# Optimization experiments

Hardware: AMD Instinct MI355X
Metric: run time of the kernel (lower is better)

## Reference

```python
import jax, jax.numpy as jnp
import numpy as np

N_NODES = 100000
N_EDGES = 1600000
N_GRAPHS = 4096
HID = 512
OUT_DIM = 12


def setup_inputs() -> dict:
    key = jax.random.key(0)
    ks = jax.random.split(key, 16)
    x = jax.random.normal(ks[0], (N_NODES, 7), dtype=jnp.float32)
    edge_index = jax.random.randint(ks[1], (2, N_EDGES), 0, N_NODES, dtype=jnp.int32)
    batch = jnp.sort(jax.random.randint(ks[2], (N_NODES,), 0, N_GRAPHS, dtype=jnp.int32))

    def lin(k, i, o):
        s = 1.0 / np.sqrt(i)
        kw, kb = jax.random.split(k)
        return (jax.random.uniform(kw, (i, o), jnp.float32, -s, s),
                jax.random.uniform(kb, (o,), jnp.float32, -s, s))

    c1_w1, c1_b1 = lin(ks[3], 7, HID)
    c1_w2, c1_b2 = lin(ks[4], HID, HID)
    c2_w1, c2_b1 = lin(ks[5], HID, HID)
    c2_w2, c2_b2 = lin(ks[6], HID, HID)
    c3_w1, c3_b1 = lin(ks[7], HID, HID)
    c3_w2, c3_b2 = lin(ks[8], HID, HID)
    lin_w1, lin_b1 = lin(ks[9], HID, 256)
    lin_w2, lin_b2 = lin(ks[10], 256, OUT_DIM)
    return dict(x=x, edge_index=edge_index, batch=batch,
                c1_w1=c1_w1, c1_b1=c1_b1, c1_w2=c1_w2, c1_b2=c1_b2,
                c2_w1=c2_w1, c2_b1=c2_b1, c2_w2=c2_w2, c2_b2=c2_b2,
                c3_w1=c3_w1, c3_b1=c3_b1, c3_w2=c3_w2, c3_b2=c3_b2,
                lin_w1=lin_w1, lin_b1=lin_b1, lin_w2=lin_w2, lin_b2=lin_b2)


def _gin_conv(x, src, dst, w1, b1, w2, b2):
    # GINConv (eps=0): h_i = mlp(x_i + sum_{j in N(i)} x_j)
    agg = jax.ops.segment_sum(x[src], dst, num_segments=N_NODES)
    h = x + agg
    h = jax.nn.relu(h @ w1 + b1) @ w2 + b2
    return h


def reference(x, edge_index, batch,
              c1_w1, c1_b1, c1_w2, c1_b2,
              c2_w1, c2_b1, c2_w2, c2_b2,
              c3_w1, c3_b1, c3_w2, c3_b2,
              lin_w1, lin_b1, lin_w2, lin_b2):
    src, dst = edge_index[0], edge_index[1]
    h = jax.nn.relu(_gin_conv(x, src, dst, c1_w1, c1_b1, c1_w2, c1_b2))
    h = jax.nn.relu(_gin_conv(h, src, dst, c2_w1, c2_b1, c2_w2, c2_b2))
    h = jax.nn.relu(_gin_conv(h, src, dst, c3_w1, c3_b1, c3_w2, c3_b2))
    # global mean pool over graphs in batch
    sums = jax.ops.segment_sum(h, batch, num_segments=N_GRAPHS)
    cnts = jax.ops.segment_sum(jnp.ones((h.shape[0],), h.dtype), batch, num_segments=N_GRAPHS)
    pooled = sums / jnp.maximum(cnts, 1.0)[:, None]
    return jax.nn.relu(pooled @ lin_w1 + lin_b1) @ lin_w2 + lin_b2
```

## Files before the change

### kernel.cpp

```cpp
#include <hip/hip_runtime.h>
#include <hip/hip_bf16.h>
#include <cstddef>
#include <cstdint>

#define N_NODES   100000
#define M_PAD     100096
#define N_EDGES   1600000
#define N_GRAPHS  4096
#define HID       512
#define OUT_DIM   12

typedef unsigned short u16;
typedef __attribute__((ext_vector_type(8))) short bf16x8;
typedef __attribute__((ext_vector_type(4))) float f32x4;

__device__ inline float bf2f(u16 u) {
    union { uint32_t i; float f; } v; v.i = (uint32_t)u << 16; return v.f;
}
__device__ inline u16 f2bf(float f) {
    union { float f; uint32_t i; } v; v.f = f;
    uint32_t r = v.i + 0x7FFFu + ((v.i >> 16) & 1u);
    return (u16)(r >> 16);
}

__device__ inline void load8_bf(const u16* p, float o[8]) {
    uint4 u = *(const uint4*)p;
    uint32_t w[4] = {u.x, u.y, u.z, u.w};
    #pragma unroll
    for (int i = 0; i < 4; ++i) {
        o[2*i]   = bf2f((u16)(w[i] & 0xFFFFu));
        o[2*i+1] = bf2f((u16)(w[i] >> 16));
    }
}
__device__ inline void store8_bf(u16* p, const float o[8]) {
    uint4 u;
    u.x = (uint32_t)f2bf(o[0]) | ((uint32_t)f2bf(o[1]) << 16);
    u.y = (uint32_t)f2bf(o[2]) | ((uint32_t)f2bf(o[3]) << 16);
    u.z = (uint32_t)f2bf(o[4]) | ((uint32_t)f2bf(o[5]) << 16);
    u.w = (uint32_t)f2bf(o[6]) | ((uint32_t)f2bf(o[7]) << 16);
    *(uint4*)p = u;
}

__global__ void zero_ints(int* __restrict__ p, int n) {
    int i = blockIdx.x * blockDim.x + threadIdx.x;
    if (i < n) p[i] = 0;
}

__global__ void hist_kernel(const int* __restrict__ dst, int* __restrict__ counts) {
    int e = blockIdx.x * blockDim.x + threadIdx.x;
    if (e < N_EDGES) atomicAdd(&counts[dst[e]], 1);
}

__global__ __launch_bounds__(1024) void scan_single(const int* __restrict__ counts,
                                                    int* __restrict__ row_start) {
    __shared__ int smem[1024];
    __shared__ int running;
    int tid = threadIdx.x;
    if (tid == 0) { running = 0; row_start[0] = 0; }
    __syncthreads();
    for (int base = 0; base < N_NODES; base += 1024) {
        int i = base + tid;
        int v = (i < N_NODES) ? counts[i] : 0;
        smem[tid] = v;
        __syncthreads();
        for (int off = 1; off < 1024; off <<= 1) {
            int t = (tid >= off) ? smem[tid - off] : 0;
            __syncthreads();
            smem[tid] += t;
            __syncthreads();
        }
        int incl = smem[tid];
        int tot  = smem[1023];
        int roff = running;
        if (i < N_NODES) row_start[i + 1] = roff + incl;
        __syncthreads();
        if (tid == 0) running = roff + tot;
        __syncthreads();
    }
}

__global__ void cursor_init(const int* __restrict__ row_start, int* __restrict__ cursor) {
    int i = blockIdx.x * blockDim.x + threadIdx.x;
    if (i < N_NODES) cursor[i] = row_start[i];
}

__global__ void scatter_edges(const int* __restrict__ src, const int* __restrict__ dst,
                              int* __restrict__ cursor, int* __restrict__ sorted_src) {
    int e = blockIdx.x * blockDim.x + threadIdx.x;
    if (e < N_EDGES) {
        int p = atomicAdd(&cursor[dst[e]], 1);
        p = min(max(p, 0), N_EDGES - 1);
        sorted_src[p] = src[e];
    }
}

__global__ __launch_bounds__(256) void transpose_to_bf16(const float* __restrict__ W,
                                                         u16* __restrict__ Wt) {
    __shared__ float t[32][33];
    int bx = blockIdx.x * 32, by = blockIdx.y * 32;
    int tx = threadIdx.x & 31, ty = threadIdx.x >> 5;
    #pragma unroll
    for (int i = 0; i < 32; i += 8)
        t[ty + i][tx] = W[(size_t)(by + ty + i) * HID + bx + tx];
    __syncthreads();
    #pragma unroll
    for (int i = 0; i < 32; i += 8)
        Wt[(size_t)(bx + ty + i) * HID + by + tx] = f2bf(t[tx][ty + i]);
}

__global__ __launch_bounds__(64) void agg7_kernel(const float* __restrict__ x,
                                                  const int* __restrict__ row_start,
                                                  const int* __restrict__ sorted_src,
                                                  float* __restrict__ out) {
    int node = blockIdx.x * 8 + (threadIdx.x >> 3);
    int d = threadIdx.x & 7;
    if (node >= N_NODES || d >= 7) return;
    float acc = x[(size_t)node * 7 + d];
    int e0 = min(row_start[node], N_EDGES);
    int e1 = min(row_start[node + 1], N_EDGES);
    for (int e = e0; e < e1; ++e) {
        unsigned si = min((unsigned)sorted_src[e], (unsigned)(N_NODES - 1));
        acc += x[(size_t)si * 7 + d];
    }
    out[(size_t)node * 7 + d] = acc;
}

__global__ __launch_bounds__(256) void agg_full(const u16* __restrict__ X,
                                                const int* __restrict__ row_start,
                                                const int* __restrict__ sorted_src,
                                                u16* __restrict__ Out) {
    int node = blockIdx.x * 4 + (threadIdx.x >> 6);
    if (node >= N_NODES) return;
    int lane = threadIdx.x & 63;
    float acc[8];
    load8_bf(X + (size_t)node * HID + lane * 8, acc);
    int e0 = min(row_start[node], N_EDGES);
    int e1 = min(row_start[node + 1], N_EDGES);
    for (int e = e0; e < e1; ++e) {
        unsigned si = min((unsigned)sorted_src[e], (unsigned)(N_NODES - 1));
        float v[8];
        load8_bf(X + (size_t)si * HID + lane * 8, v);
        #pragma unroll
        for (int k = 0; k < 8; ++k) acc[k] += v[k];
    }
    store8_bf(Out + (size_t)node * HID + lane * 8, acc);
}

__global__ __launch_bounds__(256) void gemm_k7_relu(const float* __restrict__ A7,
                                                    const float* __restrict__ W,
                                                    const float* __restrict__ bias,
                                                    u16* __restrict__ C) {
    int n = blockIdx.x;
    __shared__ float a[8];
    if (threadIdx.x < 7) a[threadIdx.x] = A7[(size_t)n * 7 + threadIdx.x];
    __syncthreads();
    for (int j = threadIdx.x; j < HID; j += 256) {
        float s = bias[j];
        #pragma unroll
        for (int k = 0; k < 7; ++k) s = fmaf(a[k], W[k * HID + j], s);
        C[(size_t)n * HID + j] = f2bf(fmaxf(s, 0.f));
    }
}

#define LDSP 40

template <bool RELU>
__global__ __launch_bounds__(256) void gemm_mfma_bf16(const u16* __restrict__ A,
                                                      const u16* __restrict__ Wt,
                                                      const float* __restrict__ bias,
                                                      u16* __restrict__ C) {
    __shared__ u16 As[128][LDSP];
    __shared__ u16 Bs[128][LDSP];
    const int tid  = threadIdx.x;
    const int wid  = tid >> 6;
    const int lane = tid & 63;
    const int wr = wid >> 1, wc = wid & 1;
    const int row0 = blockIdx.y * 128;
    const int col0 = blockIdx.x * 128;
    const int l15 = lane & 15;
    const int l4  = lane >> 4;

    f32x4 acc[4][4] = {};

    for (int k0 = 0; k0 < HID; k0 += 32) {
        #pragma unroll
        for (int i = 0; i < 2; ++i) {
            int c = tid + i * 256;
            int r = c >> 2, kc = (c & 3) * 8;
            *(uint4*)&As[r][kc] = *(const uint4*)&A [(size_t)(row0 + r) * HID + k0 + kc];
            *(uint4*)&Bs[r][kc] = *(const uint4*)&Wt[(size_t)(col0 + r) * HID + k0 + kc];
        }
        __syncthreads();
        bf16x8 af[4], bfr[4];
        #pragma unroll
        for (int m = 0; m < 4; ++m)
            af[m] = *(const bf16x8*)&As[wr * 64 + m * 16 + l15][l4 * 8];
        #pragma unroll
        for (int n = 0; n < 4; ++n)
            bfr[n] = *(const bf16x8*)&Bs[wc * 64 + n * 16 + l15][l4 * 8];
        #pragma unroll
        for (int m = 0; m < 4; ++m)
            #pragma unroll
            for (int n = 0; n < 4; ++n)
                acc[m][n] = __builtin_amdgcn_mfma_f32_16x16x32_bf16(af[m], bfr[n],
                                                                    acc[m][n], 0, 0, 0);
        __syncthreads();
    }

    #pragma unroll
    for (int m = 0; m < 4; ++m) {
        #pragma unroll
        for (int n = 0; n < 4; ++n) {
            int col = col0 + wc * 64 + n * 16 + l15;
            float b = bias[col];
            #pragma unroll
            for (int i = 0; i < 4; ++i) {
                int r = row0 + wr * 64 + m * 16 + l4 * 4 + i;
                float v = acc[m][n][i] + b;
                if (RELU) v = fmaxf(v, 0.f);
                C[(size_t)r * HID + col] = f2bf(v);
            }
        }
    }
}

template <bool RELU>
__global__ __launch_bounds__(256) void gemm_tiled_f32(const float* __restrict__ A,
                                                      const float* __restrict__ W,
                                                      const float* __restrict__ bias,
                                                      float* __restrict__ C,
                                                      int M, int N, int K) {
    __shared__ float As[16][68];
    __shared__ float Bs[16][68];
    int tid = threadIdx.x;
    int tx = tid & 15, ty = tid >> 4;
    int col0 = blockIdx.x * 64;
    int row0 = blockIdx.y * 64;
    float acc[4][4] = {};

    for (int k0 = 0; k0 < K; k0 += 16) {
        {
            int r = tid >> 2, c = (tid & 3) * 4;
            float4 v = make_float4(0.f, 0.f, 0.f, 0.f);
            int gr = row0 + r;
            if (gr < M) v = *reinterpret_cast<const float4*>(A + (size_t)gr * K + k0 + c);
            As[c + 0][r] = v.x; As[c + 1][r] = v.y; As[c + 2][r] = v.z; As[c + 3][r] = v.w;
        }
        {
            int r = tid >> 4, c = (tid & 15) * 4;
            int gc = col0 + c;
            float4 v = make_float4(0.f, 0.f, 0.f, 0.f);
            const float* wp = W + (size_t)(k0 + r) * N + gc;
            if (gc + 3 < N) {
                v = *reinterpret_cast<const float4*>(wp);
            } else {
                float t0 = (gc + 0 < N) ? wp[0] : 0.f;
                float t1 = (gc + 1 < N) ? wp[1] : 0.f;
                float t2 = (gc + 2 < N) ? wp[2] : 0.f;
                v = make_float4(t0, t1, t2, 0.f);
            }
            *reinterpret_cast<float4*>(&Bs[r][c]) = v;
        }
        __syncthreads();
        #pragma unroll
        for (int k = 0; k < 16; ++k) {
            float a[4], b[4];
            *(float4*)a = *(const float4*)&As[k][ty * 4];
            *(float4*)b = *(const float4*)&Bs[k][tx * 4];
            #pragma unroll
            for (int i = 0; i < 4; ++i)
                #pragma unroll
                for (int j = 0; j < 4; ++j)
                    acc[i][j] = fmaf(a[i], b[j], acc[i][j]);
        }
        __syncthreads();
    }

    #pragma unroll
    for (int i = 0; i < 4; ++i) {
        int r = row0 + ty * 4 + i;
        if (r >= M) break;
        #pragma unroll
        for (int j = 0; j < 4; ++j) {
            int cidx = col0 + tx * 4 + j;
            if (cidx >= N) continue;
            float v = acc[i][j] + bias[cidx];
            if (RELU) v = fmaxf(v, 0.f);
            C[(size_t)r * N + cidx] = v;
        }
    }
}

__global__ void graph_bounds(const int* __restrict__ batch, int* __restrict__ g_start) {
    int g = blockIdx.x * blockDim.x + threadIdx.x;
    if (g > N_GRAPHS) return;
    int lo = 0, hi = N_NODES;
    while (lo < hi) {
        int mid = (lo + hi) >> 1;
        if (batch[mid] < g) lo = mid + 1; else hi = mid;
    }
    g_start[g] = lo;
}

__global__ __launch_bounds__(256) void pool_kernel(const u16* __restrict__ H,
                                                   const int* __restrict__ g_start,
                                                   float* __restrict__ pooled) {
    int g = blockIdx.x * 4 + (threadIdx.x >> 6);
    if (g >= N_GRAPHS) return;
    int lane = threadIdx.x & 63;
    int s = g_start[g], e = g_start[g + 1];
    float acc[8] = {};
    for (int n = s; n < e; ++n) {
        float v[8];
        load8_bf(H + (size_t)n * HID + lane * 8, v);
        #pragma unroll
        for (int k = 0; k < 8; ++k) acc[k] += v[k];
    }
    float inv = 1.f / fmaxf((float)(e - s), 1.f);
    float* o = pooled + (size_t)g * HID + lane * 8;
    #pragma unroll
    for (int k = 0; k < 8; ++k) o[k] = acc[k] * inv;
}

__global__ void diag_kernel(float* __restrict__ out, int n, float v) {
    int i = blockIdx.x * blockDim.x + threadIdx.x;
    if (i < n) out[i] = v;
}

static inline size_t rnd256(size_t b) { return (b + 255) & ~(size_t)255; }

extern "C" void kernel_launch(void* const* d_in, const int* in_sizes, int n_in,
                              void* d_out, int out_size, void* d_ws, size_t ws_size,
                              hipStream_t stream) {
    (void)in_sizes; (void)n_in;
    const float* x     = (const float*)d_in[0];
    const int*   ei    = (const int*)d_in[1];
    const int*   batch = (const int*)d_in[2];
    const int* src = ei;
    const int* dst = ei + N_EDGES;

    const float* c1_w1 = (const float*)d_in[3];
    const float* c1_b1 = (const float*)d_in[4];
    const float* c1_w2 = (const float*)d_in[5];
    const float* c1_b2 = (const float*)d_in[6];
    const float* c2_w1 = (const float*)d_in[7];
    const float* c2_b1 = (const float*)d_in[8];
    const float* c2_w2 = (const float*)d_in[9];
    const float* c2_b2 = (const float*)d_in[10];
    const float* c3_w1 = (const float*)d_in[11];
    const float* c3_b1 = (const float*)d_in[12];
    const float* c3_w2 = (const float*)d_in[13];
    const float* c3_b2 = (const float*)d_in[14];
    const float* lin_w1 = (const float*)d_in[15];
    const float* lin_b1 = (const float*)d_in[16];
    const float* lin_w2 = (const float*)d_in[17];
    const float* lin_b2 = (const float*)d_in[18];
    float* out = (float*)d_out;

    size_t off = 0;
    auto alloc = [&](size_t bytes) -> void* {
        void* p = (char*)d_ws + off;
        off += rnd256(bytes);
        return p;
    };
    u16*   b0        = (u16*)alloc((size_t)M_PAD * HID * 2);
    u16*   b1        = (u16*)alloc((size_t)M_PAD * HID * 2);
    float* agg7buf   = (float*)alloc((size_t)N_NODES * 7 * 4);
    int*   counts    = (int*)alloc((size_t)N_NODES * 4);
    int*   cursor    = (int*)alloc((size_t)N_NODES * 4);
    int*   row_start = (int*)alloc((size_t)(N_NODES + 1) * 4);
    int*   sorted_src= (int*)alloc((size_t)N_EDGES * 4);
    int*   g_start   = (int*)alloc((size_t)(N_GRAPHS + 1) * 4);
    float* pooled    = (float*)alloc((size_t)N_GRAPHS * HID * 4);
    char*  hh_slot   = (char*)alloc((size_t)N_GRAPHS * 256 * 4);
    float* hh        = (float*)hh_slot;
    u16*   wt        = (u16*)hh_slot;
    u16* c1w2T = wt + 0 * HID * HID;
    u16* c2w1T = wt + 1 * HID * HID;
    u16* c2w2T = wt + 2 * HID * HID;
    u16* c3w1T = wt + 3 * HID * HID;
    u16* c3w2T = wt + 4 * HID * HID;

    if (off > ws_size) {
        diag_kernel<<<(out_size + 255) / 256, 256, 0, stream>>>(
            out, out_size, (float)(ws_size >> 20));
        return;
    }

    zero_ints<<<(N_NODES + 255) / 256, 256, 0, stream>>>(counts, N_NODES);
    hist_kernel<<<(N_EDGES + 255) / 256, 256, 0, stream>>>(dst, counts);
    scan_single<<<1, 1024, 0, stream>>>(counts, row_start);
    cursor_init<<<(N_NODES + 255) / 256, 256, 0, stream>>>(row_start, cursor);
    scatter_edges<<<(N_EDGES + 255) / 256, 256, 0, stream>>>(src, dst, cursor, sorted_src);
    graph_bounds<<<(N_GRAPHS + 256) / 256, 256, 0, stream>>>(batch, g_start);

    dim3 tgrid(HID / 32, HID / 32);
    transpose_to_bf16<<<tgrid, 256, 0, stream>>>(c1_w2, c1w2T);
    transpose_to_bf16<<<tgrid, 256, 0, stream>>>(c2_w1, c2w1T);
    transpose_to_bf16<<<tgrid, 256, 0, stream>>>(c2_w2, c2w2T);
    transpose_to_bf16<<<tgrid, 256, 0, stream>>>(c3_w1, c3w1T);
    transpose_to_bf16<<<tgrid, 256, 0, stream>>>(c3_w2, c3w2T);

    dim3 mgrid(HID / 128, M_PAD / 128);

    agg7_kernel<<<(N_NODES + 7) / 8, 64, 0, stream>>>(x, row_start, sorted_src, agg7buf);
    gemm_k7_relu<<<N_NODES, 256, 0, stream>>>(agg7buf, c1_w1, c1_b1, b0);
    gemm_mfma_bf16<true><<<mgrid, 256, 0, stream>>>(b0, c1w2T, c1_b2, b1);
    agg_full<<<N_NODES / 4, 256, 0, stream>>>(b1, row_start, sorted_src, b0);
    gemm_mfma_bf16<true><<<mgrid, 256, 0, stream>>>(b0, c2w1T, c2_b1, b1);
    gemm_mfma_bf16<true><<<mgrid, 256, 0, stream>>>(b1, c2w2T, c2_b2, b0);
    agg_full<<<N_NODES / 4, 256, 0, stream>>>(b0, row_start, sorted_src, b1);
    gemm_mfma_bf16<true><<<mgrid, 256, 0, stream>>>(b1, c3w1T, c3_b1, b0);
    gemm_mfma_bf16<true><<<mgrid, 256, 0, stream>>>(b0, c3w2T, c3_b2, b1);
    pool_kernel<<<N_GRAPHS / 4, 256, 0, stream>>>(b1, g_start, pooled);
    gemm_tiled_f32<true><<<dim3(256 / 64, N_GRAPHS / 64), 256, 0, stream>>>(
        pooled, lin_w1, lin_b1, hh, N_GRAPHS, 256, HID);
    gemm_tiled_f32<false><<<dim3(1, N_GRAPHS / 64), 256, 0, stream>>>(
        hh, lin_w2, lin_b2, out, N_GRAPHS, OUT_DIM, 256);
}
```

Measured before the change: 1.686 ms.

## Parallelize scan, split aggregation by column half, tile k7 GEMM, use direct-to-LDS loads

New measurement: 1.613 ms. -4.3%, faster.

```diff
diff --git a/kernel.cpp b/kernel.cpp
--- a/kernel.cpp
+++ b/kernel.cpp
@@ -41,6 +41,13 @@
     *(uint4*)p = u;
 }
 
+__device__ inline void gld16(const void* g, void* l) {
+    __builtin_amdgcn_global_load_lds(
+        (const __attribute__((address_space(1))) void*)g,
+        (__attribute__((address_space(3))) void*)(uint32_t)(uintptr_t)l,
+        16, 0, 0);
+}
+
 __global__ void zero_ints(int* __restrict__ p, int n) {
     int i = blockIdx.x * blockDim.x + threadIdx.x;
     if (i < n) p[i] = 0;
@@ -51,32 +58,43 @@
     if (e < N_EDGES) atomicAdd(&counts[dst[e]], 1);
 }
 
-__global__ __launch_bounds__(1024) void scan_single(const int* __restrict__ counts,
-                                                    int* __restrict__ row_start) {
+#define SCAN_NB 98
+
+__global__ __launch_bounds__(1024) void scan_chunks(const int* __restrict__ counts,
+                                                    int* __restrict__ row_start,
+                                                    int* __restrict__ partials) {
     __shared__ int smem[1024];
-    __shared__ int running;
     int tid = threadIdx.x;
-    if (tid == 0) { running = 0; row_start[0] = 0; }
+    int i = blockIdx.x * 1024 + tid;
+    int v = (i < N_NODES) ? counts[i] : 0;
+    smem[tid] = v;
     __syncthreads();
-    for (int base = 0; base < N_NODES; base += 1024) {
-        int i = base + tid;
-        int v = (i < N_NODES) ? counts[i] : 0;
-        smem[tid] = v;
-        __syncthreads();
-        for (int off = 1; off < 1024; off <<= 1) {
-            int t = (tid >= off) ? smem[tid - off] : 0;
-            __syncthreads();
-            smem[tid] += t;
-            __syncthreads();
-        }
-        int incl = smem[tid];
-        int tot  = smem[1023];
-        int roff = running;
-        if (i < N_NODES) row_start[i + 1] = roff + incl;
-        __syncthreads();
-        if (tid == 0) running = roff + tot;
-        __syncthreads();
-    }
+    for (int off = 1; off < 1024; off <<= 1) {
+        int t = (tid >= off) ? smem[tid - off] : 0;
+        __syncthreads();
+        smem[tid] += t;
+        __syncthreads();
+    }
+    if (i < N_NODES) row_start[i + 1] = smem[tid];
+    if (tid == 1023) partials[blockIdx.x] = smem[1023];
+}
+
+__global__ void scan_partials(int* __restrict__ partials) {
+    if (threadIdx.x == 0 && blockIdx.x == 0) {
+        int run = 0;
+        for (int b = 0; b < SCAN_NB; ++b) {
+            int t = partials[b];
+            partials[b] = run;
+            run += t;
+        }
+    }
+}
+
+__global__ __launch_bounds__(1024) void scan_add_offsets(int* __restrict__ row_start,
+                                                         const int* __restrict__ partials) {
+    int i = blockIdx.x * 1024 + threadIdx.x;
+    if (i == 0) row_start[0] = 0;
+    if (i < N_NODES) row_start[i + 1] += partials[blockIdx.x];
 }
 
 __global__ void cursor_init(const int* __restrict__ row_start, int* __restrict__ cursor) {
@@ -106,6 +124,33 @@
     #pragma unroll
     for (int i = 0; i < 32; i += 8)
         Wt[(size_t)(bx + ty + i) * HID + by + tx] = f2bf(t[tx][ty + i]);
+}
+
+template <int HALF>
+__global__ __launch_bounds__(256) void agg_half(const u16* __restrict__ X,
+                                                const int* __restrict__ row_start,
+                                                const int* __restrict__ sorted_src,
+                                                u16* __restrict__ Out) {
+    int node = blockIdx.x * 4 + (threadIdx.x >> 6);
+    int lane = threadIdx.x & 63;
+    size_t col = HALF * 256 + lane * 4;
+    uint2 s = *(const uint2*)(X + (size_t)node * HID + col);
+    float a0 = bf2f((u16)(s.x & 0xFFFFu)), a1 = bf2f((u16)(s.x >> 16));
+    float a2 = bf2f((u16)(s.y & 0xFFFFu)), a3 = bf2f((u16)(s.y >> 16));
+    int e0 = min(row_start[node], N_EDGES);
+    int e1 = min(row_start[node + 1], N_EDGES);
+    for (int e = e0; e < e1; ++e) {
+        unsigned si = min((unsigned)sorted_src[e], (unsigned)(N_NODES - 1));
+        uint2 v = *(const uint2*)(X + (size_t)si * HID + col);
+        a0 += bf2f((u16)(v.x & 0xFFFFu)); a1 += bf2f((u16)(v.x >> 16));
+        a2 += bf2f((u16)(v.y & 0xFFFFu)); a3 += bf2f((u16)(v.y >> 16));
+    }
+    uint2 o;
+    o.x = (uint32_t)f2bf(a0) | ((uint32_t)f2bf(a1) << 16);
+    o.y = (uint32_t)f2bf(a2) | ((uint32_t)f2bf(a3) << 16);
+    unsigned long long packed = (unsigned long long)o.x | ((unsigned long long)o.y << 32);
+    __builtin_nontemporal_store(packed,
+        (unsigned long long*)(Out + (size_t)node * HID + col));
 }
 
 __global__ __launch_bounds__(64) void agg7_kernel(const float* __restrict__ x,
@@ -125,52 +170,50 @@
     out[(size_t)node * 7 + d] = acc;
 }
 
-__global__ __launch_bounds__(256) void agg_full(const u16* __restrict__ X,
-                                                const int* __restrict__ row_start,
-                                                const int* __restrict__ sorted_src,
-                                                u16* __restrict__ Out) {
-    int node = blockIdx.x * 4 + (threadIdx.x >> 6);
-    if (node >= N_NODES) return;
-    int lane = threadIdx.x & 63;
-    float acc[8];
-    load8_bf(X + (size_t)node * HID + lane * 8, acc);
-    int e0 = min(row_start[node], N_EDGES);
-    int e1 = min(row_start[node + 1], N_EDGES);
-    for (int e = e0; e < e1; ++e) {
-        unsigned si = min((unsigned)sorted_src[e], (unsigned)(N_NODES - 1));
-        float v[8];
-        load8_bf(X + (size_t)si * HID + lane * 8, v);
-        #pragma unroll
-        for (int k = 0; k < 8; ++k) acc[k] += v[k];
-    }
-    store8_bf(Out + (size_t)node * HID + lane * 8, acc);
-}
-
 __global__ __launch_bounds__(256) void gemm_k7_relu(const float* __restrict__ A7,
                                                     const float* __restrict__ W,
                                                     const float* __restrict__ bias,
                                                     u16* __restrict__ C) {
-    int n = blockIdx.x;
-    __shared__ float a[8];
-    if (threadIdx.x < 7) a[threadIdx.x] = A7[(size_t)n * 7 + threadIdx.x];
+    __shared__ float Wl[7 * HID];
+    __shared__ float Bi[HID];
+    __shared__ float A7l[128 * 7];
+    int tid = threadIdx.x;
+    int node0 = blockIdx.x * 128;
+    for (int t = tid; t < 7 * HID; t += 256) Wl[t] = W[t];
+    for (int t = tid; t < HID; t += 256) Bi[t] = bias[t];
+    for (int t = tid; t < 128 * 7; t += 256) {
+        int gi = node0 * 7 + t;
+        A7l[t] = (gi < N_NODES * 7) ? A7[gi] : 0.f;
+    }
     __syncthreads();
-    for (int j = threadIdx.x; j < HID; j += 256) {
-        float s = bias[j];
-        #pragma unroll
-        for (int k = 0; k < 7; ++k) s = fmaf(a[k], W[k * HID + j], s);
-        C[(size_t)n * HID + j] = f2bf(fmaxf(s, 0.f));
-    }
-}
-
-#define LDSP 40
+    int wid = tid >> 6, lane = tid & 63;
+    for (int it = 0; it < 32; ++it) {
+        int nl = it * 4 + wid;
+        int node = node0 + nl;
+        if (node >= N_NODES) break;
+        float a[7];
+        #pragma unroll
+        for (int k = 0; k < 7; ++k) a[k] = A7l[nl * 7 + k];
+        float s[8];
+        int c0 = lane * 8;
+        #pragma unroll
+        for (int c = 0; c < 8; ++c) {
+            float v = Bi[c0 + c];
+            #pragma unroll
+            for (int k = 0; k < 7; ++k) v = fmaf(a[k], Wl[k * HID + c0 + c], v);
+            s[c] = fmaxf(v, 0.f);
+        }
+        store8_bf(C + (size_t)node * HID + c0, s);
+    }
+}
 
 template <bool RELU>
 __global__ __launch_bounds__(256) void gemm_mfma_bf16(const u16* __restrict__ A,
                                                       const u16* __restrict__ Wt,
                                                       const float* __restrict__ bias,
                                                       u16* __restrict__ C) {
-    __shared__ u16 As[128][LDSP];
-    __shared__ u16 Bs[128][LDSP];
+    __shared__ u16 As[128][32];
+    __shared__ u16 Bs[128][32];
     const int tid  = threadIdx.x;
     const int wid  = tid >> 6;
     const int lane = tid & 63;
@@ -180,15 +223,18 @@
     const int l15 = lane & 15;
     const int l4  = lane >> 4;
 
+    const int srow = lane >> 2;
+    const int scol = (lane & 3) * 8;
+
     f32x4 acc[4][4] = {};
 
     for (int k0 = 0; k0 < HID; k0 += 32) {
+        const u16* Ag = A  + (size_t)(row0 + wid * 32) * HID + k0;
+        const u16* Bg = Wt + (size_t)(col0 + wid * 32) * HID + k0;
         #pragma unroll
         for (int i = 0; i < 2; ++i) {
-            int c = tid + i * 256;
-            int r = c >> 2, kc = (c & 3) * 8;
-            *(uint4*)&As[r][kc] = *(const uint4*)&A [(size_t)(row0 + r) * HID + k0 + kc];
-            *(uint4*)&Bs[r][kc] = *(const uint4*)&Wt[(size_t)(col0 + r) * HID + k0 + kc];
+            gld16(Ag + (size_t)(i * 16 + srow) * HID + scol, &As[wid * 32 + i * 16][0]);
+            gld16(Bg + (size_t)(i * 16 + srow) * HID + scol, &Bs[wid * 32 + i * 16][0]);
         }
         __syncthreads();
         bf16x8 af[4], bfr[4];
@@ -371,6 +417,7 @@
     int*   row_start = (int*)alloc((size_t)(N_NODES + 1) * 4);
     int*   sorted_src= (int*)alloc((size_t)N_EDGES * 4);
     int*   g_start   = (int*)alloc((size_t)(N_GRAPHS + 1) * 4);
+    int*   partials  = (int*)alloc((size_t)SCAN_NB * 4);
     float* pooled    = (float*)alloc((size_t)N_GRAPHS * HID * 4);
     char*  hh_slot   = (char*)alloc((size_t)N_GRAPHS * 256 * 4);
     float* hh        = (float*)hh_slot;
@@ -389,7 +436,9 @@
 
     zero_ints<<<(N_NODES + 255) / 256, 256, 0, stream>>>(counts, N_NODES);
     hist_kernel<<<(N_EDGES + 255) / 256, 256, 0, stream>>>(dst, counts);
-    scan_single<<<1, 1024, 0, stream>>>(counts, row_start);
+    scan_chunks<<<SCAN_NB, 1024, 0, stream>>>(counts, row_start, partials);
+    scan_partials<<<1, 64, 0, stream>>>(partials);
+    scan_add_offsets<<<SCAN_NB, 1024, 0, stream>>>(row_start, partials);
     cursor_init<<<(N_NODES + 255) / 256, 256, 0, stream>>>(row_start, cursor);
     scatter_edges<<<(N_EDGES + 255) / 256, 256, 0, stream>>>(src, dst, cursor, sorted_src);
     graph_bounds<<<(N_GRAPHS + 256) / 256, 256, 0, stream>>>(batch, g_start);
@@ -402,14 +451,17 @@
     transpose_to_bf16<<<tgrid, 256, 0, stream>>>(c3_w2, c3w2T);
 
     dim3 mgrid(HID / 128, M_PAD / 128);
+    const int aggGrid = N_NODES / 4;
 
     agg7_kernel<<<(N_NODES + 7) / 8, 64, 0, stream>>>(x, row_start, sorted_src, agg7buf);
-    gemm_k7_relu<<<N_NODES, 256, 0, stream>>>(agg7buf, c1_w1, c1_b1, b0);
+    gemm_k7_relu<<<(N_NODES + 127) / 128, 256, 0, stream>>>(agg7buf, c1_w1, c1_b1, b0);
     gemm_mfma_bf16<true><<<mgrid, 256, 0, stream>>>(b0, c1w2T, c1_b2, b1);
-    agg_full<<<N_NODES / 4, 256, 0, stream>>>(b1, row_start, sorted_src, b0);
+    agg_half<0><<<aggGrid, 256, 0, stream>>>(b1, row_start, sorted_src, b0);
+    agg_half<1><<<aggGrid, 256, 0, stream>>>(b1, row_start, sorted_src, b0);
     gemm_mfma_bf16<true><<<mgrid, 256, 0, stream>>>(b0, c2w1T, c2_b1, b1);
     gemm_mfma_bf16<true><<<mgrid, 256, 0, stream>>>(b1, c2w2T, c2_b2, b0);
-    agg_full<<<N_NODES / 4, 256, 0, stream>>>(b0, row_start, sorted_src, b1);
+    agg_half<0><<<aggGrid, 256, 0, stream>>>(b0, row_start, sorted_src, b1);
+    agg_half<1><<<aggGrid, 256, 0, stream>>>(b0, row_start, sorted_src, b1);
     gemm_mfma_bf16<true><<<mgrid, 256, 0, stream>>>(b1, c3w1T, c3_b1, b0);
     gemm_mfma_bf16<true><<<mgrid, 256, 0, stream>>>(b0, c3w2T, c3_b2, b1);
     pool_kernel<<<N_GRAPHS / 4, 256, 0, stream>>>(b1, g_start, pooled);
```
